# Kernel optimization log

Hardware: AMD Instinct MI355X
Metric: run time of the kernel (lower is better)

The kernel has to match this reference:

```python
import jax, jax.numpy as jnp
import numpy as np

B, C, N = 8, 256, 2048

def setup_inputs() -> dict:
    key = jax.random.key(0)
    ks = jax.random.split(key, 7)
    s = 1.0 / np.sqrt(C)
    return {
        "x": jax.random.normal(ks[0], (B, C, N), dtype=jnp.float32),
        "Wq": jax.random.normal(ks[1], (C, C), dtype=jnp.float32) * s,
        "bq": jax.random.normal(ks[2], (C,), dtype=jnp.float32) * s,
        "Wk": jax.random.normal(ks[3], (C, C), dtype=jnp.float32) * s,
        "bk": jax.random.normal(ks[4], (C,), dtype=jnp.float32) * s,
        "Wv": jax.random.normal(ks[5], (C, C), dtype=jnp.float32) * s,
        "bv": jax.random.normal(ks[6], (C,), dtype=jnp.float32) * s,
    }

def reference(x, Wq, bq, Wk, bk, Wv, bv):
    # x: [B, C, N]; Conv1d(k=1) == channel-mixing matmul + bias
    q = jnp.einsum('oc,bcn->bon', Wq, x) + bq[None, :, None]  # [B,C,N]
    k = jnp.einsum('oc,bcn->bon', Wk, x) + bk[None, :, None]  # [B,C,N]
    v = jnp.einsum('oc,bcn->bon', Wv, x) + bv[None, :, None]  # [B,C,N]
    # qk = bmm(q^T, k): [B, N, N]
    qk = jnp.einsum('bcn,bcm->bnm', q, k)
    # global-sum normalization over the ENTIRE qk tensor (not row-wise softmax)
    attn_w = qk / jnp.sum(qk)
    # attn = bmm(v, attn_w): [B, C, N]
    attn = jnp.einsum('bcn,bnm->bcm', v, attn_w)
    return attn
```

## Files before the change

### kernel.cpp

```cpp
#include <hip/hip_runtime.h>


typedef _Float16 half8 __attribute__((ext_vector_type(8)));
typedef _Float16 half4 __attribute__((ext_vector_type(4)));
typedef float f4v __attribute__((ext_vector_type(4)));

#define GP 40

__launch_bounds__(256)
__global__ void pre_gemmG(const float* __restrict__ x, float* __restrict__ sxpart,
                          float* __restrict__ S, _Float16* __restrict__ xTh,
                          _Float16* __restrict__ xTl, float* __restrict__ Gpart) {
    extern __shared__ __align__(16) char smem[];
    const int blk = blockIdx.x, t = threadIdx.x;

    if (blk < 192) {
        _Float16* Ah = (_Float16*)smem;
        _Float16* Al = Ah + 128 * GP;
        _Float16* Bh = Al + 128 * GP;
        _Float16* Bl = Bh + 128 * GP;

        const int tileId = blk % 3;
        const int y = blk / 3;
        const int b  = y >> 3;
        const int ks = y & 7;
        const int r0 = (tileId == 2) ? 128 : 0;
        const int c0 = (tileId == 0) ? 0 : 128;
        const bool diag = (tileId != 1);
        const float* xb = x + (long)b * 524288;

        const int lane = t & 63, wave = t >> 6;
        const int wy = wave >> 1, wx = wave & 1;
        const int mIn = lane & 15, quad = lane >> 4;

        f4v acc[4][4] = {};
        const int aBase = (wy * 64 + mIn) * GP + quad * 8;
        const int bBase = (wx * 64 + mIn) * GP + quad * 8;
        const int srow = t >> 3;
        const int skq  = (t & 7) * 4;

        float4 pa[4], pb[4];
        int kk = ks * 256;
        #pragma unroll
        for (int i = 0; i < 4; ++i) {
            pa[i] = *(const float4*)&xb[(long)(r0 + srow + i * 32) * 2048 + kk + skq];
            if (!diag) pb[i] = *(const float4*)&xb[(long)(c0 + srow + i * 32) * 2048 + kk + skq];
        }

        for (int kb = 0; kb < 8; ++kb) {
            if (kb) __syncthreads();
            #pragma unroll
            for (int i = 0; i < 4; ++i) {
                const int row = srow + i * 32;
                half4 hv, lv;
                hv[0] = (_Float16)pa[i].x; lv[0] = (_Float16)(pa[i].x - (float)hv[0]);
                hv[1] = (_Float16)pa[i].y; lv[1] = (_Float16)(pa[i].y - (float)hv[1]);
                hv[2] = (_Float16)pa[i].z; lv[2] = (_Float16)(pa[i].z - (float)hv[2]);
                hv[3] = (_Float16)pa[i].w; lv[3] = (_Float16)(pa[i].w - (float)hv[3]);
                *(half4*)&Ah[row * GP + skq] = hv;
                *(half4*)&Al[row * GP + skq] = lv;
                if (!diag) {
                    half4 hb, lb;
                    hb[0] = (_Float16)pb[i].x; lb[0] = (_Float16)(pb[i].x - (float)hb[0]);
                    hb[1] = (_Float16)pb[i].y; lb[1] = (_Float16)(pb[i].y - (float)hb[1]);
                    hb[2] = (_Float16)pb[i].z; lb[2] = (_Float16)(pb[i].z - (float)hb[2]);
                    hb[3] = (_Float16)pb[i].w; lb[3] = (_Float16)(pb[i].w - (float)hb[3]);
                    *(half4*)&Bh[row * GP + skq] = hb;
                    *(half4*)&Bl[row * GP + skq] = lb;
                }
            }
            __syncthreads();
            kk += 32;
            if (kb < 7) {
                #pragma unroll
                for (int i = 0; i < 4; ++i) {
                    pa[i] = *(const float4*)&xb[(long)(r0 + srow + i * 32) * 2048 + kk + skq];
                    if (!diag) pb[i] = *(const float4*)&xb[(long)(c0 + srow + i * 32) * 2048 + kk + skq];
                }
            }
            const _Float16* BhP = diag ? Ah : Bh;
            const _Float16* BlP = diag ? Al : Bl;
            #pragma unroll
            for (int ph = 0; ph < 3; ++ph) {
                const _Float16* As = (ph == 2) ? Al : Ah;
                const _Float16* Bs = (ph == 1) ? BlP : BhP;
                half8 af[4], bf[4];
                #pragma unroll
                for (int i = 0; i < 4; ++i) {
                    af[i] = *(const half8*)&As[aBase + i * 16 * GP];
                    bf[i] = *(const half8*)&Bs[bBase + i * 16 * GP];
                }
                #pragma unroll
                for (int i = 0; i < 4; ++i)
                    #pragma unroll
                    for (int j = 0; j < 4; ++j)
                        acc[i][j] = __builtin_amdgcn_mfma_f32_16x16x32_f16(af[i], bf[j], acc[i][j], 0, 0, 0);
            }
        }

        float* D = Gpart + ((long)(ks * 8 + b) << 16);
        #pragma unroll
        for (int i = 0; i < 4; ++i)
            #pragma unroll
            for (int j = 0; j < 4; ++j) {
                const int row = r0 + wy * 64 + i * 16 + quad * 4;
                const int col = c0 + wx * 64 + j * 16 + mIn;
                #pragma unroll
                for (int r = 0; r < 4; ++r)
                    D[(row + r) * 256 + col] = acc[i][j][r];
                if (tileId == 1)
                    *(float4*)&D[(long)col * 256 + row] =
                        make_float4(acc[i][j][0], acc[i][j][1], acc[i][j][2], acc[i][j][3]);
            }
    } else {
        if (blk == 192 && t == 0) S[0] = 0.0f;
        float* tl  = (float*)smem;
        float* red = (float*)(smem + 16640);
        const int tile = blk - 192;
        const int b  = tile >> 7;
        const int tb = tile & 127;
        const int ntile = tb & 31;
        const int n0 = ntile * 64;
        const int c0 = (tb >> 5) * 64;
        const float* xb = x + (long)b * 524288;
        #pragma unroll
        for (int p = 0; p < 16; ++p) {
            const int idx = t + p * 256;
            const int r = idx >> 6, c = idx & 63;
            tl[r * 65 + c] = xb[(long)(c0 + r) * 2048 + n0 + c];
        }
        __syncthreads();
        #pragma unroll
        for (int p = 0; p < 16; ++p) {
            const int idx = t + p * 256;
            const int n = idx >> 6, c = idx & 63;
            const float v = tl[c * 65 + n];
            const _Float16 h = (_Float16)v;
            const _Float16 l = (_Float16)(v - (float)h);
            const long o = (long)b * 524288 + (long)(n0 + n) * 256 + c0 + c;
            xTh[o] = h; xTl[o] = l;
        }
        const int c = t & 63, q = t >> 6;
        float s = 0.0f;
        #pragma unroll
        for (int k = 0; k < 16; ++k) s += tl[c * 65 + q * 16 + k];
        red[t] = s; __syncthreads();
        if (t < 64)
            sxpart[ntile * 2048 + b * 256 + c0 + t] =
                red[t] + red[t + 64] + red[t + 128] + red[t + 192];
    }
}

__launch_bounds__(256)
__global__ void prep1_kernel(const float* __restrict__ Wq, const float* __restrict__ Wk,
                             const float* __restrict__ Wv, const float* __restrict__ bq,
                             const float* __restrict__ bk, const float* __restrict__ sxpart,
                             float* __restrict__ W3, float* __restrict__ u2,
                             float* __restrict__ w1, float* __restrict__ s1,
                             float* __restrict__ wvsx, float* __restrict__ tq) {
    const int blk = blockIdx.x, t = threadIdx.x;
    if (blk < 16) {
        const int r0 = (blk >> 2) * 64, j0 = (blk & 3) * 64;
        __shared__ float ldsA[16 * 68], ldsB[16 * 68];
        const int tx = t & 15, ty = t >> 4;
        float acc[4][4] = {};
        for (int kk = 0; kk < 256; kk += 16) {
            *(float4*)&ldsA[ty * 68 + tx * 4] = *(const float4*)&Wq[(long)(kk + ty) * 256 + r0 + tx * 4];
            *(float4*)&ldsB[ty * 68 + tx * 4] = *(const float4*)&Wk[(long)(kk + ty) * 256 + j0 + tx * 4];
            __syncthreads();
            #pragma unroll
            for (int k = 0; k < 16; ++k) {
                const float4 av4 = *(const float4*)&ldsA[k * 68 + ty * 4];
                const float4 bv4 = *(const float4*)&ldsB[k * 68 + tx * 4];
                const float ar[4] = {av4.x, av4.y, av4.z, av4.w};
                const float br[4] = {bv4.x, bv4.y, bv4.z, bv4.w};
                #pragma unroll
                for (int i = 0; i < 4; ++i)
                    #pragma unroll
                    for (int j = 0; j < 4; ++j)
                        acc[i][j] = fmaf(ar[i], br[j], acc[i][j]);
            }
            __syncthreads();
        }
        #pragma unroll
        for (int i = 0; i < 4; ++i)
            *(float4*)&W3[(long)(r0 + ty * 4 + i) * 256 + j0 + tx * 4] =
                make_float4(acc[i][0], acc[i][1], acc[i][2], acc[i][3]);
    } else if (blk == 16) {
        __shared__ float sbq[256], sbk[256], red[256];
        sbq[t] = bq[t]; sbk[t] = bk[t];
        __syncthreads();
        float u = 0.0f, w = 0.0f;
        #pragma unroll 8
        for (int c = 0; c < 256; ++c) {
            u = fmaf(Wk[(long)c * 256 + t], sbq[c], u);
            w = fmaf(Wq[(long)c * 256 + t], sbk[c], w);
        }
        u2[t] = u; w1[t] = w;
        red[t] = sbq[t] * sbk[t]; __syncthreads();
        for (int h = 128; h > 0; h >>= 1) { if (t < h) red[t] += red[t + h]; __syncthreads(); }
        if (t == 0) s1[0] = red[0];
    } else {
        const int sel = blk - 17;
        const bool isTq = sel >= 4;
        const float* M = isTq ? Wq : Wv;
        const int r0w = (sel & 3) * 64;
        __shared__ float wtile[64 * 256];
        __shared__ float sxs[2048];
        #pragma unroll
        for (int p = 0; p < 16; ++p) {
            const int idx = t + p * 256;
            const int row = idx >> 6, f4 = idx & 63;
            *(float4*)&wtile[row * 256 + f4 * 4] = *(const float4*)&M[(long)(r0w + row) * 256 + f4 * 4];
        }
        #pragma unroll
        for (int p = 0; p < 8; ++p) {
            const int idx = t + p * 256;
            float s = 0.0f;
            for (int nt = 0; nt < 32; ++nt) s += sxpart[nt * 2048 + idx];
            sxs[idx] = s;
        }
        __syncthreads();
        const int r = t >> 2, q = t & 3;
        float acc[8] = {};
        for (int ci = 0; ci < 64; ++ci) {
            const float wv = wtile[r * 256 + q * 64 + ci];
            #pragma unroll
            for (int b = 0; b < 8; ++b) acc[b] = fmaf(wv, sxs[b * 256 + q * 64 + ci], acc[b]);
        }
        #pragma unroll
        for (int b = 0; b < 8; ++b) {
            acc[b] += __shfl_xor(acc[b], 1);
            acc[b] += __shfl_xor(acc[b], 2);
        }
        if (q == 0) {
            if (isTq) {
                const float bias = 2048.0f * bq[r0w + r];
                #pragma unroll
                for (int b = 0; b < 8; ++b) tq[b * 256 + r0w + r] = acc[b] + bias;
            } else {
                #pragma unroll
                for (int b = 0; b < 8; ++b) wvsx[b * 256 + r0w + r] = acc[b];
            }
        }
    }
}

__launch_bounds__(256)
__global__ void t1_kernel(const float* __restrict__ Wv, const float* __restrict__ Gpart,
                          const float* __restrict__ Wk, const float* __restrict__ bk,
                          const float* __restrict__ bv, const float* __restrict__ tq,
                          const float* __restrict__ sxpart, const float* __restrict__ s1p,
                          const float* __restrict__ wvsx, const float* __restrict__ w1,
                          float* __restrict__ T1, float* __restrict__ tdot,
                          float* __restrict__ v2, float* __restrict__ cvecInit,
                          float* __restrict__ S) {
    const int blk = blockIdx.x, t = threadIdx.x;
    if (blk < 128) {
        __shared__ float ldsA[16 * 68], ldsB[16 * 68];
        const int j0s = blk & 3;
        const int j0 = j0s * 64;
        const int r0 = ((blk >> 2) & 3) * 64;
        const int b = blk >> 4;
        const int tx = t & 15, ty = t >> 4;
        const int sr = t >> 2, sk = (t & 3) * 4;
        float acc[4][4] = {};
        for (int kk = 0; kk < 256; kk += 16) {
            const float4 a4 = *(const float4*)&Wv[(long)(r0 + sr) * 256 + kk + sk];
            ldsA[(sk + 0) * 68 + sr] = a4.x;
            ldsA[(sk + 1) * 68 + sr] = a4.y;
            ldsA[(sk + 2) * 68 + sr] = a4.z;
            ldsA[(sk + 3) * 68 + sr] = a4.w;
            float4 bs = make_float4(0.f, 0.f, 0.f, 0.f);
            #pragma unroll
            for (int ksl = 0; ksl < 8; ++ksl) {
                const float4 g = *(const float4*)&Gpart[(long)ksl * 524288 + (long)b * 65536 +
                                                        (long)(kk + ty) * 256 + j0 + tx * 4];
                bs.x += g.x; bs.y += g.y; bs.z += g.z; bs.w += g.w;
            }
            *(float4*)&ldsB[ty * 68 + tx * 4] = bs;
            __syncthreads();
            #pragma unroll
            for (int k = 0; k < 16; ++k) {
                const float4 av4 = *(const float4*)&ldsA[k * 68 + ty * 4];
                const float4 bv4 = *(const float4*)&ldsB[k * 68 + tx * 4];
                const float ar[4] = {av4.x, av4.y, av4.z, av4.w};
                const float br[4] = {bv4.x, bv4.y, bv4.z, bv4.w};
                #pragma unroll
                for (int i = 0; i < 4; ++i)
                    #pragma unroll
                    for (int j = 0; j < 4; ++j)
                        acc[i][j] = fmaf(ar[i], br[j], acc[i][j]);
            }
            __syncthreads();
        }
        float* D = T1 + (long)b * 65536;
        float w4[4];
        *(float4*)w4 = *(const float4*)&w1[j0 + tx * 4];
        #pragma unroll
        for (int i = 0; i < 4; ++i) {
            const int r = r0 + ty * 4 + i;
            *(float4*)&D[(long)r * 256 + j0 + tx * 4] =
                make_float4(acc[i][0], acc[i][1], acc[i][2], acc[i][3]);
            float p = acc[i][0] * w4[0] + acc[i][1] * w4[1] + acc[i][2] * w4[2] + acc[i][3] * w4[3];
            p += __shfl_xor(p, 1); p += __shfl_xor(p, 2);
            p += __shfl_xor(p, 4); p += __shfl_xor(p, 8);
            if (tx == 0) tdot[j0s * 2048 + b * 256 + r] = p;
        }
    } else {
        const int b = blk - 128, j = t;
        __shared__ float ssx[256], stq[256], red[256];
        float s = 0.0f;
        for (int nt = 0; nt < 32; ++nt) s += sxpart[nt * 2048 + b * 256 + j];
        ssx[j] = s;
        stq[j] = tq[b * 256 + j];
        __syncthreads();
        float vr = 0.0f;
        #pragma unroll 8
        for (int c = 0; c < 256; ++c) vr = fmaf(Wk[(long)c * 256 + j], stq[c], vr);
        v2[b * 256 + j] = vr;
        __shared__ float sd1;
        red[j] = vr * ssx[j]; __syncthreads();
        for (int h = 128; h > 0; h >>= 1) { if (j < h) red[j] += red[j + h]; __syncthreads(); }
        if (j == 0) sd1 = red[0];
        __syncthreads();
        red[j] = stq[j] * bk[j]; __syncthreads();
        for (int h = 128; h > 0; h >>= 1) { if (j < h) red[j] += red[j + h]; __syncthreads(); }
        const float s2v = red[0];
        if (j == 0) atomicAdd(S, sd1 + 2048.0f * s2v);
        cvecInit[b * 256 + j] = wvsx[b * 256 + j] * s1p[0] + bv[j] * s2v;
    }
}

__launch_bounds__(256)
__global__ void ap_kernel(const float* __restrict__ T1, const float* __restrict__ W3,
                          const float* __restrict__ wvsx, const float* __restrict__ u2,
                          const float* __restrict__ bv, const float* __restrict__ v2,
                          _Float16* __restrict__ Aph, _Float16* __restrict__ Apl) {
    __shared__ float ldsA[16 * 68], ldsB[16 * 68];
    const int b = blockIdx.z;
    const int r0 = blockIdx.y * 64, j0 = blockIdx.x * 64;
    const float* A = T1 + (long)b * 65536;
    const int t = threadIdx.x, tx = t & 15, ty = t >> 4;
    const int sr = t >> 2, sk = (t & 3) * 4;
    float acc[4][4] = {};
    for (int kk = 0; kk < 256; kk += 16) {
        const float4 a4 = *(const float4*)&A[(long)(r0 + sr) * 256 + kk + sk];
        ldsA[(sk + 0) * 68 + sr] = a4.x;
        ldsA[(sk + 1) * 68 + sr] = a4.y;
        ldsA[(sk + 2) * 68 + sr] = a4.z;
        ldsA[(sk + 3) * 68 + sr] = a4.w;
        *(float4*)&ldsB[ty * 68 + tx * 4] = *(const float4*)&W3[(long)(kk + ty) * 256 + j0 + tx * 4];
        __syncthreads();
        #pragma unroll
        for (int k = 0; k < 16; ++k) {
            const float4 av4 = *(const float4*)&ldsA[k * 68 + ty * 4];
            const float4 bv4 = *(const float4*)&ldsB[k * 68 + tx * 4];
            const float ar[4] = {av4.x, av4.y, av4.z, av4.w};
            const float br[4] = {bv4.x, bv4.y, bv4.z, bv4.w};
            #pragma unroll
            for (int i = 0; i < 4; ++i)
                #pragma unroll
                for (int j = 0; j < 4; ++j)
                    acc[i][j] = fmaf(ar[i], br[j], acc[i][j]);
        }
        __syncthreads();
    }
    #pragma unroll
    for (int i = 0; i < 4; ++i) {
        const int r = r0 + ty * 4 + i;
        const float e1 = wvsx[b * 256 + r], e3 = bv[r];
        half4 hv, lv;
        #pragma unroll
        for (int j = 0; j < 4; ++j) {
            const int col = j0 + tx * 4 + j;
            const float val = acc[i][j] + e1 * u2[col] + e3 * v2[b * 256 + col];
            hv[j] = (_Float16)val;
            lv[j] = (_Float16)(val - (float)hv[j]);
        }
        const long o = (long)b * 65536 + (long)r * 256 + j0 + tx * 4;
        *(half4*)&Aph[o] = hv;
        *(half4*)&Apl[o] = lv;
    }
}

__launch_bounds__(256)
__global__ void gemmF_mfma(const _Float16* __restrict__ Aph, const _Float16* __restrict__ Apl,
                           const _Float16* __restrict__ xTh, const _Float16* __restrict__ xTl,
                           const float* __restrict__ Sptr, const float* __restrict__ cvecInit,
                           const float* __restrict__ tdot, float* __restrict__ out) {
    __shared__ __align__(16) _Float16 Ah[128 * GP];
    __shared__ __align__(16) _Float16 Al[128 * GP];
    __shared__ __align__(16) _Float16 Bh[128 * GP];
    __shared__ __align__(16) _Float16 Bl[128 * GP];

    const int n0 = blockIdx.x * 128;
    const int c0 = blockIdx.y * 128;
    const int b = blockIdx.z;
    const _Float16* Asrc_h = Aph + (long)b * 65536;
    const _Float16* Asrc_l = Apl + (long)b * 65536;
    const _Float16* Bsrc_h = xTh + (long)b * 524288;
    const _Float16* Bsrc_l = xTl + (long)b * 524288;

    const int t = threadIdx.x;
    const int lane = t & 63, wave = t >> 6;
    const int wy = wave >> 1, wx = wave & 1;
    const int mIn = lane & 15, quad = lane >> 4;

    f4v acc[4][4] = {};
    const int aBase = (wy * 64 + mIn) * GP + quad * 8;
    const int bBase = (wx * 64 + mIn) * GP + quad * 8;

    for (int kk = 0; kk < 256; kk += 32) {
        #pragma unroll
        for (int i = 0; i < 2; ++i) {
            const int idx = t + (i << 8);
            const int row = idx >> 2, ko = (idx & 3) << 3;
            *(uint4*)&Ah[row * GP + ko] = *(const uint4*)&Asrc_h[(long)(c0 + row) * 256 + kk + ko];
            *(uint4*)&Al[row * GP + ko] = *(const uint4*)&Asrc_l[(long)(c0 + row) * 256 + kk + ko];
            *(uint4*)&Bh[row * GP + ko] = *(const uint4*)&Bsrc_h[(long)(n0 + row) * 256 + kk + ko];
            *(uint4*)&Bl[row * GP + ko] = *(const uint4*)&Bsrc_l[(long)(n0 + row) * 256 + kk + ko];
        }
        __syncthreads();
        #pragma unroll
        for (int ph = 0; ph < 3; ++ph) {
            const _Float16* As = (ph == 2) ? Al : Ah;
            const _Float16* Bs = (ph == 1) ? Bl : Bh;
            half8 af[4], bf[4];
            #pragma unroll
            for (int i = 0; i < 4; ++i) {
                af[i] = *(const half8*)&As[aBase + i * 16 * GP];
                bf[i] = *(const half8*)&Bs[bBase + i * 16 * GP];
            }
            #pragma unroll
            for (int i = 0; i < 4; ++i)
                #pragma unroll
                for (int j = 0; j < 4; ++j)
                    acc[i][j] = __builtin_amdgcn_mfma_f32_16x16x32_f16(af[i], bf[j], acc[i][j], 0, 0, 0);
        }
        __syncthreads();
    }

    const float invS = 1.0f / Sptr[0];
    float* ob = out + (long)b * 524288;
    #pragma unroll
    for (int i = 0; i < 4; ++i)
        #pragma unroll
        for (int r = 0; r < 4; ++r) {
            const int row = c0 + wy * 64 + i * 16 + quad * 4 + r;
            const int ci = b * 256 + row;
            const float c = cvecInit[ci] + tdot[ci] + tdot[2048 + ci] +
                            tdot[4096 + ci] + tdot[6144 + ci];
            #pragma unroll
            for (int j = 0; j < 4; ++j) {
                const int col = n0 + wx * 64 + j * 16 + mIn;
                ob[(long)row * 2048 + col] = (acc[i][j][r] + c) * invS;
            }
        }
}

extern "C" void kernel_launch(void* const* d_in, const int* in_sizes, int n_in,
                              void* d_out, int out_size, void* d_ws, size_t ws_size,
                              hipStream_t stream) {
    const float* x  = (const float*)d_in[0];
    const float* Wq = (const float*)d_in[1];
    const float* bq = (const float*)d_in[2];
    const float* Wk = (const float*)d_in[3];
    const float* bk = (const float*)d_in[4];
    const float* Wv = (const float*)d_in[5];
    const float* bv = (const float*)d_in[6];
    float* out = (float*)d_out;
    float* ws  = (float*)d_ws;

    const int B = 8;
    float* T1     = ws;
    float* W3     = ws + 524288;
    float* sxpart = ws + 589824;
    float* wvsx   = ws + 655360;
    float* v2     = ws + 657408;
    float* cvecI  = ws + 659456;
    float* tq     = ws + 661504;
    float* tdot   = ws + 663552;
    float* u2     = ws + 671744;
    float* w1     = ws + 672000;
    float* s1     = ws + 672256;
    float* S      = ws + 672260;
    float* Gpart  = ws + 672288;
    _Float16* fh  = (_Float16*)(ws + 4866592);
    _Float16* xTh = fh;
    _Float16* xTl = fh + 4194304;
    _Float16* Aph = fh + 8388608;
    _Float16* Apl = fh + 8912896;

    pre_gemmG<<<dim3(1216), 256, 40960, stream>>>(x, sxpart, S, xTh, xTl, Gpart);
    prep1_kernel<<<dim3(25), 256, 0, stream>>>(Wq, Wk, Wv, bq, bk, sxpart,
                                               W3, u2, w1, s1, wvsx, tq);
    t1_kernel<<<dim3(136), 256, 0, stream>>>(Wv, Gpart, Wk, bk, bv, tq, sxpart, s1,
                                             wvsx, w1, T1, tdot, v2, cvecI, S);
    ap_kernel<<<dim3(4, 4, B), 256, 0, stream>>>(T1, W3, wvsx, u2, bv, v2, Aph, Apl);
    gemmF_mfma<<<dim3(16, 2, B), 256, 0, stream>>>(Aph, Apl, xTh, xTl, S, cvecI, tdot, out);
}
```

Measured before the change: 158.2 us.

## Drop transposed fp16 x copy, split x in final GEMM, merge prep kernels

Removes the pre-pass that wrote transposed hi/lo fp16 copies of x. The final GEMM now loads fp32 x tiles directly, transposes them through LDS and does the hi/lo split in place. Row sums of x are folded into the Gram GEMM, which now uses fewer, longer k-splits (96 blocks instead of 192). The prep work is regrouped into fewer launches, with the bias-vector dot product moved into ap_kernel. This saves a large memory round-trip and one launch, at the cost of less parallelism in the Gram GEMM and extra LDS transpose work inside the final GEMM.

After: 155.5 us. Within noise of the previous version (-1.7%).

```diff
diff --git a/kernel.cpp b/kernel.cpp
--- a/kernel.cpp
+++ b/kernel.cpp
@@ -3,27 +3,29 @@
 
 typedef _Float16 half8 __attribute__((ext_vector_type(8)));
 typedef _Float16 half4 __attribute__((ext_vector_type(4)));
+typedef _Float16 half2v __attribute__((ext_vector_type(2)));
 typedef float f4v __attribute__((ext_vector_type(4)));
 
-#define GP 40
+#define GP  40
+#define GPB 36
 
 __launch_bounds__(256)
-__global__ void pre_gemmG(const float* __restrict__ x, float* __restrict__ sxpart,
-                          float* __restrict__ S, _Float16* __restrict__ xTh,
-                          _Float16* __restrict__ xTl, float* __restrict__ Gpart) {
-    extern __shared__ __align__(16) char smem[];
+__global__ void k1_kernel(const float* __restrict__ x, const float* __restrict__ Wq,
+                          const float* __restrict__ Wk, const float* __restrict__ bq,
+                          const float* __restrict__ bk, float* __restrict__ sxpart,
+                          float* __restrict__ W3, float* __restrict__ u2,
+                          float* __restrict__ w1, float* __restrict__ s1,
+                          float* __restrict__ S, float* __restrict__ Gpart) {
+    __shared__ __align__(16) char smem[40960];
     const int blk = blockIdx.x, t = threadIdx.x;
-
-    if (blk < 192) {
+    if (blk < 96) {
         _Float16* Ah = (_Float16*)smem;
         _Float16* Al = Ah + 128 * GP;
         _Float16* Bh = Al + 128 * GP;
         _Float16* Bl = Bh + 128 * GP;
-
         const int tileId = blk % 3;
         const int y = blk / 3;
-        const int b  = y >> 3;
-        const int ks = y & 7;
+        const int b = y >> 2, ks = y & 3;
         const int r0 = (tileId == 2) ? 128 : 0;
         const int c0 = (tileId == 0) ? 0 : 128;
         const bool diag = (tileId != 1);
@@ -38,16 +40,17 @@
         const int bBase = (wx * 64 + mIn) * GP + quad * 8;
         const int srow = t >> 3;
         const int skq  = (t & 7) * 4;
+        float rs[4] = {};
 
         float4 pa[4], pb[4];
-        int kk = ks * 256;
+        int kk = ks * 512;
         #pragma unroll
         for (int i = 0; i < 4; ++i) {
             pa[i] = *(const float4*)&xb[(long)(r0 + srow + i * 32) * 2048 + kk + skq];
             if (!diag) pb[i] = *(const float4*)&xb[(long)(c0 + srow + i * 32) * 2048 + kk + skq];
         }
 
-        for (int kb = 0; kb < 8; ++kb) {
+        for (int kb = 0; kb < 16; ++kb) {
             if (kb) __syncthreads();
             #pragma unroll
             for (int i = 0; i < 4; ++i) {
@@ -59,7 +62,9 @@
                 hv[3] = (_Float16)pa[i].w; lv[3] = (_Float16)(pa[i].w - (float)hv[3]);
                 *(half4*)&Ah[row * GP + skq] = hv;
                 *(half4*)&Al[row * GP + skq] = lv;
-                if (!diag) {
+                if (diag) {
+                    rs[i] += pa[i].x + pa[i].y + pa[i].z + pa[i].w;
+                } else {
                     half4 hb, lb;
                     hb[0] = (_Float16)pb[i].x; lb[0] = (_Float16)(pb[i].x - (float)hb[0]);
                     hb[1] = (_Float16)pb[i].y; lb[1] = (_Float16)(pb[i].y - (float)hb[1]);
@@ -71,7 +76,7 @@
             }
             __syncthreads();
             kk += 32;
-            if (kb < 7) {
+            if (kb < 15) {
                 #pragma unroll
                 for (int i = 0; i < 4; ++i) {
                     pa[i] = *(const float4*)&xb[(long)(r0 + srow + i * 32) * 2048 + kk + skq];
@@ -95,6 +100,20 @@
                     #pragma unroll
                     for (int j = 0; j < 4; ++j)
                         acc[i][j] = __builtin_amdgcn_mfma_f32_16x16x32_f16(af[i], bf[j], acc[i][j], 0, 0, 0);
+            }
+        }
+
+        if (diag) {
+            #pragma unroll
+            for (int i = 0; i < 4; ++i) {
+                rs[i] += __shfl_xor(rs[i], 1);
+                rs[i] += __shfl_xor(rs[i], 2);
+                rs[i] += __shfl_xor(rs[i], 4);
+            }
+            if ((t & 7) == 0) {
+                #pragma unroll
+                for (int i = 0; i < 4; ++i)
+                    sxpart[ks * 2048 + b * 256 + r0 + srow + i * 32] = rs[i];
             }
         }
 
@@ -112,56 +131,11 @@
                     *(float4*)&D[(long)col * 256 + row] =
                         make_float4(acc[i][j][0], acc[i][j][1], acc[i][j][2], acc[i][j][3]);
             }
-    } else {
-        if (blk == 192 && t == 0) S[0] = 0.0f;
-        float* tl  = (float*)smem;
-        float* red = (float*)(smem + 16640);
-        const int tile = blk - 192;
-        const int b  = tile >> 7;
-        const int tb = tile & 127;
-        const int ntile = tb & 31;
-        const int n0 = ntile * 64;
-        const int c0 = (tb >> 5) * 64;
-        const float* xb = x + (long)b * 524288;
-        #pragma unroll
-        for (int p = 0; p < 16; ++p) {
-            const int idx = t + p * 256;
-            const int r = idx >> 6, c = idx & 63;
-            tl[r * 65 + c] = xb[(long)(c0 + r) * 2048 + n0 + c];
-        }
-        __syncthreads();
-        #pragma unroll
-        for (int p = 0; p < 16; ++p) {
-            const int idx = t + p * 256;
-            const int n = idx >> 6, c = idx & 63;
-            const float v = tl[c * 65 + n];
-            const _Float16 h = (_Float16)v;
-            const _Float16 l = (_Float16)(v - (float)h);
-            const long o = (long)b * 524288 + (long)(n0 + n) * 256 + c0 + c;
-            xTh[o] = h; xTl[o] = l;
-        }
-        const int c = t & 63, q = t >> 6;
-        float s = 0.0f;
-        #pragma unroll
-        for (int k = 0; k < 16; ++k) s += tl[c * 65 + q * 16 + k];
-        red[t] = s; __syncthreads();
-        if (t < 64)
-            sxpart[ntile * 2048 + b * 256 + c0 + t] =
-                red[t] + red[t + 64] + red[t + 128] + red[t + 192];
-    }
-}
-
-__launch_bounds__(256)
-__global__ void prep1_kernel(const float* __restrict__ Wq, const float* __restrict__ Wk,
-                             const float* __restrict__ Wv, const float* __restrict__ bq,
-                             const float* __restrict__ bk, const float* __restrict__ sxpart,
-                             float* __restrict__ W3, float* __restrict__ u2,
-                             float* __restrict__ w1, float* __restrict__ s1,
-                             float* __restrict__ wvsx, float* __restrict__ tq) {
-    const int blk = blockIdx.x, t = threadIdx.x;
-    if (blk < 16) {
-        const int r0 = (blk >> 2) * 64, j0 = (blk & 3) * 64;
-        __shared__ float ldsA[16 * 68], ldsB[16 * 68];
+    } else if (blk < 112) {
+        float* ldsA = (float*)smem;
+        float* ldsB = ldsA + 16 * 68;
+        const int tile = blk - 96;
+        const int r0 = (tile >> 2) * 64, j0 = (tile & 3) * 64;
         const int tx = t & 15, ty = t >> 4;
         float acc[4][4] = {};
         for (int kk = 0; kk < 256; kk += 16) {
@@ -186,8 +160,11 @@
         for (int i = 0; i < 4; ++i)
             *(float4*)&W3[(long)(r0 + ty * 4 + i) * 256 + j0 + tx * 4] =
                 make_float4(acc[i][0], acc[i][1], acc[i][2], acc[i][3]);
-    } else if (blk == 16) {
-        __shared__ float sbq[256], sbk[256], red[256];
+    } else {
+        float* sbq = (float*)smem;
+        float* sbk = sbq + 256;
+        float* red = sbk + 256;
+        if (t == 0) S[0] = 0.0f;
         sbq[t] = bq[t]; sbk[t] = bk[t];
         __syncthreads();
         float u = 0.0f, w = 0.0f;
@@ -200,66 +177,22 @@
         red[t] = sbq[t] * sbk[t]; __syncthreads();
         for (int h = 128; h > 0; h >>= 1) { if (t < h) red[t] += red[t + h]; __syncthreads(); }
         if (t == 0) s1[0] = red[0];
-    } else {
-        const int sel = blk - 17;
-        const bool isTq = sel >= 4;
-        const float* M = isTq ? Wq : Wv;
-        const int r0w = (sel & 3) * 64;
-        __shared__ float wtile[64 * 256];
-        __shared__ float sxs[2048];
-        #pragma unroll
-        for (int p = 0; p < 16; ++p) {
-            const int idx = t + p * 256;
-            const int row = idx >> 6, f4 = idx & 63;
-            *(float4*)&wtile[row * 256 + f4 * 4] = *(const float4*)&M[(long)(r0w + row) * 256 + f4 * 4];
-        }
-        #pragma unroll
-        for (int p = 0; p < 8; ++p) {
-            const int idx = t + p * 256;
-            float s = 0.0f;
-            for (int nt = 0; nt < 32; ++nt) s += sxpart[nt * 2048 + idx];
-            sxs[idx] = s;
-        }
-        __syncthreads();
-        const int r = t >> 2, q = t & 3;
-        float acc[8] = {};
-        for (int ci = 0; ci < 64; ++ci) {
-            const float wv = wtile[r * 256 + q * 64 + ci];
-            #pragma unroll
-            for (int b = 0; b < 8; ++b) acc[b] = fmaf(wv, sxs[b * 256 + q * 64 + ci], acc[b]);
-        }
-        #pragma unroll
-        for (int b = 0; b < 8; ++b) {
-            acc[b] += __shfl_xor(acc[b], 1);
-            acc[b] += __shfl_xor(acc[b], 2);
-        }
-        if (q == 0) {
-            if (isTq) {
-                const float bias = 2048.0f * bq[r0w + r];
-                #pragma unroll
-                for (int b = 0; b < 8; ++b) tq[b * 256 + r0w + r] = acc[b] + bias;
-            } else {
-                #pragma unroll
-                for (int b = 0; b < 8; ++b) wvsx[b * 256 + r0w + r] = acc[b];
-            }
-        }
     }
 }
 
 __launch_bounds__(256)
-__global__ void t1_kernel(const float* __restrict__ Wv, const float* __restrict__ Gpart,
-                          const float* __restrict__ Wk, const float* __restrict__ bk,
-                          const float* __restrict__ bv, const float* __restrict__ tq,
-                          const float* __restrict__ sxpart, const float* __restrict__ s1p,
-                          const float* __restrict__ wvsx, const float* __restrict__ w1,
-                          float* __restrict__ T1, float* __restrict__ tdot,
-                          float* __restrict__ v2, float* __restrict__ cvecInit,
-                          float* __restrict__ S) {
+__global__ void k2_kernel(const float* __restrict__ Wv, const float* __restrict__ Gpart,
+                          const float* __restrict__ W3, const float* __restrict__ u2,
+                          const float* __restrict__ w1, const float* __restrict__ s1p,
+                          const float* __restrict__ sxpart, float* __restrict__ T1,
+                          float* __restrict__ v2, float* __restrict__ s2,
+                          float* __restrict__ wvsx, float* __restrict__ S) {
+    __shared__ __align__(16) char smem[40960];
     const int blk = blockIdx.x, t = threadIdx.x;
     if (blk < 128) {
-        __shared__ float ldsA[16 * 68], ldsB[16 * 68];
-        const int j0s = blk & 3;
-        const int j0 = j0s * 64;
+        float* ldsA = (float*)smem;
+        float* ldsB = ldsA + 16 * 68;
+        const int j0 = (blk & 3) * 64;
         const int r0 = ((blk >> 2) & 3) * 64;
         const int b = blk >> 4;
         const int tx = t & 15, ty = t >> 4;
@@ -273,7 +206,7 @@
             ldsA[(sk + 3) * 68 + sr] = a4.w;
             float4 bs = make_float4(0.f, 0.f, 0.f, 0.f);
             #pragma unroll
-            for (int ksl = 0; ksl < 8; ++ksl) {
+            for (int ksl = 0; ksl < 4; ++ksl) {
                 const float4 g = *(const float4*)&Gpart[(long)ksl * 524288 + (long)b * 65536 +
                                                         (long)(kk + ty) * 256 + j0 + tx * 4];
                 bs.x += g.x; bs.y += g.y; bs.z += g.z; bs.w += g.w;
@@ -295,40 +228,73 @@
             __syncthreads();
         }
         float* D = T1 + (long)b * 65536;
-        float w4[4];
-        *(float4*)w4 = *(const float4*)&w1[j0 + tx * 4];
-        #pragma unroll
-        for (int i = 0; i < 4; ++i) {
-            const int r = r0 + ty * 4 + i;
-            *(float4*)&D[(long)r * 256 + j0 + tx * 4] =
+        #pragma unroll
+        for (int i = 0; i < 4; ++i)
+            *(float4*)&D[(long)(r0 + ty * 4 + i) * 256 + j0 + tx * 4] =
                 make_float4(acc[i][0], acc[i][1], acc[i][2], acc[i][3]);
-            float p = acc[i][0] * w4[0] + acc[i][1] * w4[1] + acc[i][2] * w4[2] + acc[i][3] * w4[3];
-            p += __shfl_xor(p, 1); p += __shfl_xor(p, 2);
-            p += __shfl_xor(p, 4); p += __shfl_xor(p, 8);
-            if (tx == 0) tdot[j0s * 2048 + b * 256 + r] = p;
-        }
-    } else {
+    } else if (blk < 136) {
+        float* ssx = (float*)smem;
+        float* red = ssx + 256;
         const int b = blk - 128, j = t;
-        __shared__ float ssx[256], stq[256], red[256];
-        float s = 0.0f;
-        for (int nt = 0; nt < 32; ++nt) s += sxpart[nt * 2048 + b * 256 + j];
-        ssx[j] = s;
-        stq[j] = tq[b * 256 + j];
+        const float sxv = sxpart[b * 256 + j] + sxpart[2048 + b * 256 + j] +
+                          sxpart[4096 + b * 256 + j] + sxpart[6144 + b * 256 + j];
+        ssx[j] = sxv;
         __syncthreads();
         float vr = 0.0f;
         #pragma unroll 8
-        for (int c = 0; c < 256; ++c) vr = fmaf(Wk[(long)c * 256 + j], stq[c], vr);
-        v2[b * 256 + j] = vr;
-        __shared__ float sd1;
-        red[j] = vr * ssx[j]; __syncthreads();
+        for (int c = 0; c < 256; ++c) vr = fmaf(W3[(long)c * 256 + j], ssx[c], vr);
+        const float v2j = vr + 2048.0f * u2[j];
+        v2[b * 256 + j] = v2j;
+        red[j] = v2j * sxv; __syncthreads();
         for (int h = 128; h > 0; h >>= 1) { if (j < h) red[j] += red[j + h]; __syncthreads(); }
-        if (j == 0) sd1 = red[0];
-        __syncthreads();
-        red[j] = stq[j] * bk[j]; __syncthreads();
+        const float sd1 = red[0];
+        __syncthreads();
+        red[j] = sxv * w1[j]; __syncthreads();
         for (int h = 128; h > 0; h >>= 1) { if (j < h) red[j] += red[j + h]; __syncthreads(); }
-        const float s2v = red[0];
-        if (j == 0) atomicAdd(S, sd1 + 2048.0f * s2v);
-        cvecInit[b * 256 + j] = wvsx[b * 256 + j] * s1p[0] + bv[j] * s2v;
+        if (j == 0) {
+            const float s2v = red[0] + 2048.0f * s1p[0];
+            s2[b] = s2v;
+            atomicAdd(S, sd1 + 2048.0f * s2v);
+        }
+    } else {
+        float* wtile = (float*)smem;
+        float* sxs = wtile + 8192;
+        const int r0w = (blk - 136) * 32;
+        #pragma unroll
+        for (int p = 0; p < 8; ++p) {
+            const int f = t + p * 256;
+            const int row = f >> 6, c4 = f & 63;
+            *(float4*)&wtile[row * 256 + c4 * 4] = *(const float4*)&Wv[(long)(r0w + row) * 256 + c4 * 4];
+        }
+        #pragma unroll
+        for (int p = 0; p < 2; ++p) {
+            const int f = t + p * 256;
+            float4 s = make_float4(0.f, 0.f, 0.f, 0.f);
+            #pragma unroll
+            for (int ks = 0; ks < 4; ++ks) {
+                const float4 g = *(const float4*)&sxpart[ks * 2048 + f * 4];
+                s.x += g.x; s.y += g.y; s.z += g.z; s.w += g.w;
+            }
+            *(float4*)&sxs[f * 4] = s;
+        }
+        __syncthreads();
+        const int r = t >> 3, q = t & 7;
+        float acc[8] = {};
+        for (int ci = 0; ci < 32; ++ci) {
+            const float wv = wtile[r * 256 + q * 32 + ci];
+            #pragma unroll
+            for (int b = 0; b < 8; ++b) acc[b] = fmaf(wv, sxs[b * 256 + q * 32 + ci], acc[b]);
+        }
+        #pragma unroll
+        for (int b = 0; b < 8; ++b) {
+            acc[b] += __shfl_xor(acc[b], 1);
+            acc[b] += __shfl_xor(acc[b], 2);
+            acc[b] += __shfl_xor(acc[b], 4);
+        }
+        if (q == 0) {
+            #pragma unroll
+            for (int b = 0; b < 8; ++b) wvsx[b * 256 + r0w + r] = acc[b];
+        }
     }
 }
 
@@ -336,14 +302,18 @@
 __global__ void ap_kernel(const float* __restrict__ T1, const float* __restrict__ W3,
                           const float* __restrict__ wvsx, const float* __restrict__ u2,
                           const float* __restrict__ bv, const float* __restrict__ v2,
-                          _Float16* __restrict__ Aph, _Float16* __restrict__ Apl) {
-    __shared__ float ldsA[16 * 68], ldsB[16 * 68];
+                          const float* __restrict__ w1, const float* __restrict__ s1p,
+                          const float* __restrict__ s2, _Float16* __restrict__ Aph,
+                          _Float16* __restrict__ Apl, float* __restrict__ cvec) {
+    __shared__ float ldsA[16 * 68], ldsB[16 * 68], sw1[256];
     const int b = blockIdx.z;
     const int r0 = blockIdx.y * 64, j0 = blockIdx.x * 64;
     const float* A = T1 + (long)b * 65536;
     const int t = threadIdx.x, tx = t & 15, ty = t >> 4;
     const int sr = t >> 2, sk = (t & 3) * 4;
+    sw1[t] = w1[t];
     float acc[4][4] = {};
+    float dot[4] = {};
     for (int kk = 0; kk < 256; kk += 16) {
         const float4 a4 = *(const float4*)&A[(long)(r0 + sr) * 256 + kk + sk];
         ldsA[(sk + 0) * 68 + sr] = a4.x;
@@ -358,11 +328,14 @@
             const float4 bv4 = *(const float4*)&ldsB[k * 68 + tx * 4];
             const float ar[4] = {av4.x, av4.y, av4.z, av4.w};
             const float br[4] = {bv4.x, bv4.y, bv4.z, bv4.w};
-            #pragma unroll
-            for (int i = 0; i < 4; ++i)
+            const float wk = sw1[kk + k];
+            #pragma unroll
+            for (int i = 0; i < 4; ++i) {
+                dot[i] = fmaf(ar[i], wk, dot[i]);
                 #pragma unroll
                 for (int j = 0; j < 4; ++j)
                     acc[i][j] = fmaf(ar[i], br[j], acc[i][j]);
+            }
         }
         __syncthreads();
     }
@@ -381,26 +354,27 @@
         const long o = (long)b * 65536 + (long)r * 256 + j0 + tx * 4;
         *(half4*)&Aph[o] = hv;
         *(half4*)&Apl[o] = lv;
+        if (j0 == 0 && tx == 0)
+            cvec[b * 256 + r] = dot[i] + e1 * s1p[0] + e3 * s2[b];
     }
 }
 
 __launch_bounds__(256)
 __global__ void gemmF_mfma(const _Float16* __restrict__ Aph, const _Float16* __restrict__ Apl,
-                           const _Float16* __restrict__ xTh, const _Float16* __restrict__ xTl,
-                           const float* __restrict__ Sptr, const float* __restrict__ cvecInit,
-                           const float* __restrict__ tdot, float* __restrict__ out) {
+                           const float* __restrict__ x, const float* __restrict__ Sptr,
+                           const float* __restrict__ cvec, float* __restrict__ out) {
     __shared__ __align__(16) _Float16 Ah[128 * GP];
     __shared__ __align__(16) _Float16 Al[128 * GP];
-    __shared__ __align__(16) _Float16 Bh[128 * GP];
-    __shared__ __align__(16) _Float16 Bl[128 * GP];
+    __shared__ __align__(16) _Float16 Bh[128 * GPB];
+    __shared__ __align__(16) _Float16 Bl[128 * GPB];
+    __shared__ __align__(16) float xt[32 * 132];
 
     const int n0 = blockIdx.x * 128;
     const int c0 = blockIdx.y * 128;
     const int b = blockIdx.z;
     const _Float16* Asrc_h = Aph + (long)b * 65536;
     const _Float16* Asrc_l = Apl + (long)b * 65536;
-    const _Float16* Bsrc_h = xTh + (long)b * 524288;
-    const _Float16* Bsrc_l = xTl + (long)b * 524288;
+    const float* xb = x + (long)b * 524288;
 
     const int t = threadIdx.x;
     const int lane = t & 63, wave = t >> 6;
@@ -409,7 +383,9 @@
 
     f4v acc[4][4] = {};
     const int aBase = (wy * 64 + mIn) * GP + quad * 8;
-    const int bBase = (wx * 64 + mIn) * GP + quad * 8;
+    const int bBase = (wx * 64 + mIn) * GPB + quad * 8;
+    const int cn = t & 127;
+    const int ckh = (t >> 7) * 16;
 
     for (int kk = 0; kk < 256; kk += 32) {
         #pragma unroll
@@ -418,8 +394,29 @@
             const int row = idx >> 2, ko = (idx & 3) << 3;
             *(uint4*)&Ah[row * GP + ko] = *(const uint4*)&Asrc_h[(long)(c0 + row) * 256 + kk + ko];
             *(uint4*)&Al[row * GP + ko] = *(const uint4*)&Asrc_l[(long)(c0 + row) * 256 + kk + ko];
-            *(uint4*)&Bh[row * GP + ko] = *(const uint4*)&Bsrc_h[(long)(n0 + row) * 256 + kk + ko];
-            *(uint4*)&Bl[row * GP + ko] = *(const uint4*)&Bsrc_l[(long)(n0 + row) * 256 + kk + ko];
+        }
+        #pragma unroll
+        for (int p = 0; p < 4; ++p) {
+            const int f = t + p * 256;
+            const int k = f >> 5, n4 = f & 31;
+            *(float4*)&xt[k * 132 + n4 * 4] = *(const float4*)&xb[(long)(kk + k) * 2048 + n0 + n4 * 4];
+        }
+        __syncthreads();
+        {
+            _Float16 hs[16], ls[16];
+            #pragma unroll
+            for (int k = 0; k < 16; ++k) {
+                const float v = xt[(ckh + k) * 132 + cn];
+                hs[k] = (_Float16)v;
+                ls[k] = (_Float16)(v - (float)hs[k]);
+            }
+            #pragma unroll
+            for (int k2 = 0; k2 < 8; ++k2) {
+                half2v h2; h2[0] = hs[2 * k2]; h2[1] = hs[2 * k2 + 1];
+                half2v l2; l2[0] = ls[2 * k2]; l2[1] = ls[2 * k2 + 1];
+                *(half2v*)&Bh[cn * GPB + ckh + 2 * k2] = h2;
+                *(half2v*)&Bl[cn * GPB + ckh + 2 * k2] = l2;
+            }
         }
         __syncthreads();
         #pragma unroll
@@ -430,7 +427,9 @@
             #pragma unroll
             for (int i = 0; i < 4; ++i) {
                 af[i] = *(const half8*)&As[aBase + i * 16 * GP];
-                bf[i] = *(const half8*)&Bs[bBase + i * 16 * GP];
+                const half4 b0 = *(const half4*)&Bs[bBase + i * 16 * GPB];
+                const half4 b1 = *(const half4*)&Bs[bBase + i * 16 * GPB + 4];
+                bf[i] = __builtin_shufflevector(b0, b1, 0, 1, 2, 3, 4, 5, 6, 7);
             }
             #pragma unroll
             for (int i = 0; i < 4; ++i)
@@ -443,14 +442,13 @@
 
     const float invS = 1.0f / Sptr[0];
     float* ob = out + (long)b * 524288;
+    const float* cv = cvec + b * 256;
     #pragma unroll
     for (int i = 0; i < 4; ++i)
         #pragma unroll
         for (int r = 0; r < 4; ++r) {
             const int row = c0 + wy * 64 + i * 16 + quad * 4 + r;
-            const int ci = b * 256 + row;
-            const float c = cvecInit[ci] + tdot[ci] + tdot[2048 + ci] +
-                            tdot[4096 + ci] + tdot[6144 + ci];
+            const float c = cv[row];
             #pragma unroll
             for (int j = 0; j < 4; ++j) {
                 const int col = n0 + wx * 64 + j * 16 + mIn;
@@ -472,31 +470,23 @@
     float* out = (float*)d_out;
     float* ws  = (float*)d_ws;
 
-    const int B = 8;
     float* T1     = ws;
     float* W3     = ws + 524288;
     float* sxpart = ws + 589824;
-    float* wvsx   = ws + 655360;
-    float* v2     = ws + 657408;
-    float* cvecI  = ws + 659456;
-    float* tq     = ws + 661504;
-    float* tdot   = ws + 663552;
-    float* u2     = ws + 671744;
-    float* w1     = ws + 672000;
-    float* s1     = ws + 672256;
-    float* S      = ws + 672260;
-    float* Gpart  = ws + 672288;
-    _Float16* fh  = (_Float16*)(ws + 4866592);
-    _Float16* xTh = fh;
-    _Float16* xTl = fh + 4194304;
-    _Float16* Aph = fh + 8388608;
-    _Float16* Apl = fh + 8912896;
-
-    pre_gemmG<<<dim3(1216), 256, 40960, stream>>>(x, sxpart, S, xTh, xTl, Gpart);
-    prep1_kernel<<<dim3(25), 256, 0, stream>>>(Wq, Wk, Wv, bq, bk, sxpart,
-                                               W3, u2, w1, s1, wvsx, tq);
-    t1_kernel<<<dim3(136), 256, 0, stream>>>(Wv, Gpart, Wk, bk, bv, tq, sxpart, s1,
-                                             wvsx, w1, T1, tdot, v2, cvecI, S);
-    ap_kernel<<<dim3(4, 4, B), 256, 0, stream>>>(T1, W3, wvsx, u2, bv, v2, Aph, Apl);
-    gemmF_mfma<<<dim3(16, 2, B), 256, 0, stream>>>(Aph, Apl, xTh, xTl, S, cvecI, tdot, out);
+    float* wvsx   = ws + 598016;
+    float* v2     = ws + 600064;
+    float* cvec   = ws + 602112;
+    float* s2     = ws + 604160;
+    float* u2     = ws + 604168;
+    float* w1     = ws + 604424;
+    float* s1     = ws + 604680;
+    float* S      = ws + 604681;
+    float* Gpart  = ws + 604688;
+    _Float16* Aph = (_Float16*)(ws + 2701840);
+    _Float16* Apl = Aph + 524288;
+
+    k1_kernel<<<dim3(113), 256, 0, stream>>>(x, Wq, Wk, bq, bk, sxpart, W3, u2, w1, s1, S, Gpart);
+    k2_kernel<<<dim3(144), 256, 0, stream>>>(Wv, Gpart, W3, u2, w1, s1, sxpart, T1, v2, s2, wvsx, S);
+    ap_kernel<<<dim3(4, 4, 8), 256, 0, stream>>>(T1, W3, wvsx, u2, bv, v2, w1, s1, s2, Aph, Apl, cvec);
+    gemmF_mfma<<<dim3(16, 2, 8), 256, 0, stream>>>(Aph, Apl, x, S, cvec, out);
 }
```
